# Kernel optimization log

Hardware: AMD Instinct MI355X
Metric: run time of the kernel (lower is better)

## Reference

```python
import jax, jax.numpy as jnp
import numpy as np

B, T, N_EMBD, HEAD = 8, 2048, 1024, 64

def setup_inputs() -> dict:
    key = jax.random.key(0)
    kx, kk, kq, kv = jax.random.split(key, 4)
    x = jax.random.normal(kx, (B, T, N_EMBD), dtype=jnp.float32)
    Wk = jax.random.normal(kk, (HEAD, N_EMBD), dtype=jnp.float32) * 0.02
    Wq = jax.random.normal(kq, (HEAD, N_EMBD), dtype=jnp.float32) * 0.02
    Wv = jax.random.normal(kv, (HEAD, N_EMBD), dtype=jnp.float32) * 0.02
    return {"x": x, "Wk": Wk, "Wq": Wq, "Wv": Wv}

def reference(x, Wk, Wq, Wv):
    # x: [B, T, C]; Linear(n_embd, head_size, bias=False) => x @ W.T
    Bq, Tq, C = x.shape
    q = jnp.einsum('btc,hc->bth', x, Wq)  # [B, T, H]
    k = jnp.einsum('btc,hc->bth', x, Wk)
    v = jnp.einsum('btc,hc->bth', x, Wv)
    # NOTE: source scales by C**0.5 with C = n_embd (not head_size); preserved.
    scale = 1.0 / jnp.sqrt(jnp.float32(C))
    wei = jnp.einsum('bth,bsh->bts', q, k) * scale  # [B, T, T]
    # causal mask: allow key position s <= query position t
    causal = jnp.tril(jnp.ones((Tq, Tq), dtype=bool))
    wei = jnp.where(causal[None, :, :], wei, -jnp.inf)
    wei = jax.nn.softmax(wei, axis=-1)
    # dropout is identity at inference
    out = jnp.einsum('bts,bsh->bth', wei, v)  # [B, T, H]
    return out
```

## Files before the change

### kernel.cpp

```cpp
#include <hip/hip_runtime.h>

#define TB 2048
#define NB 8
#define CEMB 1024
#define HD 64
#define BT (NB*TB)
#define QSCALE 0.04508422f

typedef __attribute__((ext_vector_type(8))) short bf16x8;
typedef __attribute__((ext_vector_type(4))) short bf16x4;
typedef __attribute__((ext_vector_type(4))) float f32x4;

#define MFMA32(a, b, c) __builtin_amdgcn_mfma_f32_16x16x32_bf16(a, b, c, 0, 0, 0)
#define MFMA16(a, b, c) __builtin_amdgcn_mfma_f32_16x16x16bf16_1k(a, b, c, 0, 0, 0)

__device__ inline short f2bf(float f) {
    union { float f; unsigned u; } v; v.f = f;
    unsigned r = v.u + 0x7fffu + ((v.u >> 16) & 1u);
    return (short)(r >> 16);
}
__device__ inline float bf2f(short s) {
    union { unsigned u; float f; } v; v.u = ((unsigned)(unsigned short)s) << 16;
    return v.f;
}
__device__ inline unsigned cvt_pk_bf16(float a, float b) {
    unsigned r;
    asm("v_cvt_pk_bf16_f32 %0, %1, %2" : "=v"(r) : "v"(a), "v"(b));
    return r;
}
__device__ inline bf16x4 pack2(unsigned w0, unsigned w1) {
    union { unsigned u[2]; bf16x4 v; } c; c.u[0] = w0; c.u[1] = w1; return c.v;
}
__device__ inline bf16x8 pack4(unsigned w0, unsigned w1, unsigned w2, unsigned w3) {
    union { unsigned u[4]; bf16x8 v; } c;
    c.u[0] = w0; c.u[1] = w1; c.u[2] = w2; c.u[3] = w3; return c.v;
}
__device__ inline float bflo(unsigned w) {
    union { unsigned u; float f; } v; v.u = w << 16; return v.f;
}
__device__ inline float bfhi(unsigned w) {
    union { unsigned u; float f; } v; v.u = w & 0xffff0000u; return v.f;
}

__global__ __launch_bounds__(256) void wpack(const float* __restrict__ Wk,
                                             const float* __restrict__ Wq,
                                             const float* __restrict__ Wv,
                                             short* __restrict__ W2) {
    int c = blockIdx.x * 256 + threadIdx.x;
    int lane = c & 63, ntk = c >> 6;
    int nt = ntk % 12, kc = ntk / 12;
    int n = nt * 16 + (lane & 15);
    int col = kc * 32 + (lane >> 4) * 8;
    const float* src = (n < 64) ? Wk + n * 1024
                     : (n < 128) ? Wq + (n - 64) * 1024
                                 : Wv + (n - 128) * 1024;
    float4 a = *(const float4*)(src + col);
    float4 b = *(const float4*)(src + col + 4);
    bf16x8 o;
    o[0] = f2bf(a.x); o[1] = f2bf(a.y); o[2] = f2bf(a.z); o[3] = f2bf(a.w);
    o[4] = f2bf(b.x); o[5] = f2bf(b.y); o[6] = f2bf(b.z); o[7] = f2bf(b.w);
    *(bf16x8*)(W2 + (size_t)c * 8) = o;
}

__global__ __launch_bounds__(256, 4) void qkv_proj(const float* __restrict__ x,
                                                   const short* __restrict__ W2,
                                                   short* __restrict__ Qb,
                                                   short* __restrict__ Kb,
                                                   short* __restrict__ Vt) {
    __shared__ uint2 Lred[4][3][3][64];
    int tid = threadIdx.x, wave = tid >> 6, lane = tid & 63;
    int l15 = lane & 15, quad = lane >> 4;
    int m0 = blockIdx.x * 16;

    f32x4 acc[12];
#pragma unroll
    for (int i = 0; i < 12; ++i) acc[i] = f32x4{0.f, 0.f, 0.f, 0.f};

    const float4* xA = (const float4*)(x + (size_t)(m0 + l15) * CEMB + wave * 256) + quad * 2;
    float4 xq[4];
    xq[0] = xA[0]; xq[1] = xA[1]; xq[2] = xA[8]; xq[3] = xA[9];

    const short* wbase = W2 + ((size_t)(wave * 8) * 12 * 64 + lane) * 8;
#pragma unroll
    for (int kc = 0; kc < 8; ++kc) {
        bf16x8 wf[12];
#pragma unroll
        for (int nt = 0; nt < 12; ++nt)
            wf[nt] = *(const bf16x8*)(wbase + (size_t)kc * 6144 + nt * 512);
        int base = (kc & 1) * 2;
        float4 a0 = xq[base], a1 = xq[base + 1];
        if (kc + 2 < 8) {
            xq[base]     = xA[(kc + 2) * 8];
            xq[base + 1] = xA[(kc + 2) * 8 + 1];
        }
        bf16x8 af0 = pack4(cvt_pk_bf16(a0.x, a0.y), cvt_pk_bf16(a0.z, a0.w),
                           cvt_pk_bf16(a1.x, a1.y), cvt_pk_bf16(a1.z, a1.w));
#pragma unroll
        for (int nt = 0; nt < 12; ++nt)
            acc[nt] = MFMA32(af0, wf[nt], acc[nt]);
    }

#pragma unroll
    for (int nt = 0; nt < 12; ++nt) {
        int o = nt / 3;
        if (o != wave) {
            int rank = wave - (wave > o ? 1 : 0);
            uint2 p;
            p.x = cvt_pk_bf16(acc[nt][0], acc[nt][1]);
            p.y = cvt_pk_bf16(acc[nt][2], acc[nt][3]);
            Lred[o][rank][nt % 3][lane] = p;
        }
    }
    __syncthreads();

    int b = blockIdx.x >> 7;
    int sblk32 = (blockIdx.x & 127) >> 1;
    int half = blockIdx.x & 1;
#pragma unroll
    for (int nt = 0; nt < 12; ++nt) {
        if (wave == nt / 3) {
            f32x4 s0 = acc[nt];
#pragma unroll
            for (int rk = 0; rk < 3; ++rk) {
                uint2 p0 = Lred[nt / 3][rk][nt % 3][lane];
                s0[0] += bflo(p0.x); s0[1] += bfhi(p0.x);
                s0[2] += bflo(p0.y); s0[3] += bfhi(p0.y);
            }
            if (nt < 4) {
                int h = nt * 16 + l15;
#pragma unroll
                for (int r = 0; r < 4; ++r)
                    Kb[(size_t)(m0 + quad * 4 + r) * HD + h] = f2bf(s0[r]);
            } else if (nt < 8) {
                int h = (nt - 4) * 16 + l15;
#pragma unroll
                for (int r = 0; r < 4; ++r)
                    Qb[(size_t)(m0 + quad * 4 + r) * HD + h] = f2bf(s0[r] * QSCALE);
            } else {
                int h = (nt - 8) * 16 + l15;
                uint2 v2;
                v2.x = cvt_pk_bf16(s0[0], s0[1]);
                v2.y = cvt_pk_bf16(s0[2], s0[3]);
                *(uint2*)(Vt + ((size_t)((b * 64 + sblk32) * 64 + h)) * 32
                             + quad * 8 + half * 4) = v2;
            }
        }
    }
}

__global__ __launch_bounds__(256) void flash(const short* __restrict__ Qb,
                                             const short* __restrict__ Kb,
                                             const short* __restrict__ Vt,
                                             float* __restrict__ out) {
    __shared__ float Of[4][2][16][68];
    __shared__ float Ml[4][2][16];
    int tid = threadIdx.x, wave = tid >> 6, lane = tid & 63;
    int l15 = lane & 15, quad = lane >> 4;
    int i = blockIdx.x;
    int round = i >> 8, s = i & 255;
    int b = s & 7;
    int g32 = s >> 3;
    int q32 = round ? 63 - g32 : g32;
    int tq0 = q32 * 32;
    size_t bT = (size_t)b * TB;

    const short* qr0 = Qb + (bT + tq0 + l15) * HD;
    const short* qr1 = Qb + (bT + tq0 + 16 + l15) * HD;
    bf16x8 qf00 = *(const bf16x8*)(qr0 + quad * 8);
    bf16x8 qf01 = *(const bf16x8*)(qr0 + 32 + quad * 8);
    bf16x8 qf10 = *(const bf16x8*)(qr1 + quad * 8);
    bf16x8 qf11 = *(const bf16x8*)(qr1 + 32 + quad * 8);

    bf16x4 ones4;
#pragma unroll
    for (int j = 0; j < 4; ++j) ones4[j] = (short)0x3F80;

    f32x4 accO0[4], accO1[4];
#pragma unroll
    for (int k = 0; k < 4; ++k) { accO0[k] = f32x4{0.f,0.f,0.f,0.f}; accO1[k] = f32x4{0.f,0.f,0.f,0.f}; }
    f32x4 accL0 = f32x4{0.f,0.f,0.f,0.f}, accL1 = f32x4{0.f,0.f,0.f,0.f};

    int ntiles = (tq0 + 95) >> 6;
    const short* kbase = Kb + bT * HD;
    const short* vtb = Vt + (size_t)b * 131072;

    int myt = wave;
    if (myt < ntiles) {
        bf16x8 kf[8];
        {
            const short* kr = kbase + (size_t)(myt * 64 + l15) * HD + quad * 8;
#pragma unroll
            for (int st = 0; st < 4; ++st) {
                kf[st * 2]     = *(const bf16x8*)(kr + (size_t)st * 16 * HD);
                kf[st * 2 + 1] = *(const bf16x8*)(kr + (size_t)st * 16 * HD + 32);
            }
        }
        for (; myt < ntiles; myt += 4) {
            int s0 = myt * 64;
            bf16x8 vf8[8];
#pragma unroll
            for (int sb2 = 0; sb2 < 2; ++sb2)
#pragma unroll
                for (int ht = 0; ht < 4; ++ht)
                    vf8[sb2 * 4 + ht] = *(const bf16x8*)(
                        vtb + ((size_t)(((s0 >> 5) + sb2) * 64 + ht * 16 + l15)) * 32 + quad * 8);
            f32x4 sv0[4], sv1[4];
            __builtin_amdgcn_s_setprio(1);
#pragma unroll
            for (int st = 0; st < 4; ++st) {
                f32x4 t0 = f32x4{0.f,0.f,0.f,0.f}, t1 = f32x4{0.f,0.f,0.f,0.f};
                t0 = MFMA32(kf[st * 2], qf00, t0);
                t0 = MFMA32(kf[st * 2 + 1], qf01, t0);
                t1 = MFMA32(kf[st * 2], qf10, t1);
                t1 = MFMA32(kf[st * 2 + 1], qf11, t1);
                sv0[st] = t0; sv1[st] = t1;
            }
            __builtin_amdgcn_s_setprio(0);
            if (myt + 4 < ntiles) {
                const short* kr = kbase + (size_t)(s0 + 256 + l15) * HD + quad * 8;
#pragma unroll
                for (int st = 0; st < 4; ++st) {
                    kf[st * 2]     = *(const bf16x8*)(kr + (size_t)st * 16 * HD);
                    kf[st * 2 + 1] = *(const bf16x8*)(kr + (size_t)st * 16 * HD + 32);
                }
            }
            bf16x4 pk0[4], pk1[4];
            if (s0 + 63 <= tq0) {
#pragma unroll
                for (int st = 0; st < 4; ++st) {
                    unsigned w00 = cvt_pk_bf16(__builtin_amdgcn_exp2f(sv0[st][0]),
                                               __builtin_amdgcn_exp2f(sv0[st][1]));
                    unsigned w01 = cvt_pk_bf16(__builtin_amdgcn_exp2f(sv0[st][2]),
                                               __builtin_amdgcn_exp2f(sv0[st][3]));
                    unsigned w10 = cvt_pk_bf16(__builtin_amdgcn_exp2f(sv1[st][0]),
                                               __builtin_amdgcn_exp2f(sv1[st][1]));
                    unsigned w11 = cvt_pk_bf16(__builtin_amdgcn_exp2f(sv1[st][2]),
                                               __builtin_amdgcn_exp2f(sv1[st][3]));
                    pk0[st] = pack2(w00, w01);
                    pk1[st] = pack2(w10, w11);
                }
            } else {
                int t0g = tq0 + l15, t1g = tq0 + 16 + l15;
#pragma unroll
                for (int st = 0; st < 4; ++st) {
                    bool full0 = (s0 + st * 16 + 15 <= tq0);
                    bool full1 = (s0 + st * 16 + 15 <= tq0 + 16);
                    int sb = s0 + st * 16 + quad * 4;
                    float a0 = (full0 || sb + 0 <= t0g) ? __builtin_amdgcn_exp2f(sv0[st][0]) : 0.f;
                    float a1 = (full0 || sb + 1 <= t0g) ? __builtin_amdgcn_exp2f(sv0[st][1]) : 0.f;
                    float a2 = (full0 || sb + 2 <= t0g) ? __builtin_amdgcn_exp2f(sv0[st][2]) : 0.f;
                    float a3 = (full0 || sb + 3 <= t0g) ? __builtin_amdgcn_exp2f(sv0[st][3]) : 0.f;
                    float c0 = (full1 || sb + 0 <= t1g) ? __builtin_amdgcn_exp2f(sv1[st][0]) : 0.f;
                    float c1 = (full1 || sb + 1 <= t1g) ? __builtin_amdgcn_exp2f(sv1[st][1]) : 0.f;
                    float c2 = (full1 || sb + 2 <= t1g) ? __builtin_amdgcn_exp2f(sv1[st][2]) : 0.f;
                    float c3 = (full1 || sb + 3 <= t1g) ? __builtin_amdgcn_exp2f(sv1[st][3]) : 0.f;
                    pk0[st] = pack2(cvt_pk_bf16(a0, a1), cvt_pk_bf16(a2, a3));
                    pk1[st] = pack2(cvt_pk_bf16(c0, c1), cvt_pk_bf16(c2, c3));
                }
            }
            __builtin_amdgcn_s_setprio(1);
#pragma unroll
            for (int g = 0; g < 4; ++g) {
                accL0 = MFMA16(ones4, pk0[g], accL0);
                accL1 = MFMA16(ones4, pk1[g], accL1);
#pragma unroll
                for (int ht = 0; ht < 4; ++ht) {
                    bf16x8 v = vf8[(g >> 1) * 4 + ht];
                    bf16x4 va;
                    if (g & 1) { va[0] = v[4]; va[1] = v[5]; va[2] = v[6]; va[3] = v[7]; }
                    else       { va[0] = v[0]; va[1] = v[1]; va[2] = v[2]; va[3] = v[3]; }
                    accO0[ht] = MFMA16(va, pk0[g], accO0[ht]);
                    accO1[ht] = MFMA16(va, pk1[g], accO1[ht]);
                }
            }
            __builtin_amdgcn_s_setprio(0);
        }
    }

#pragma unroll
    for (int ht = 0; ht < 4; ++ht) {
        float4 o0, o1;
        o0.x = accO0[ht][0]; o0.y = accO0[ht][1]; o0.z = accO0[ht][2]; o0.w = accO0[ht][3];
        o1.x = accO1[ht][0]; o1.y = accO1[ht][1]; o1.z = accO1[ht][2]; o1.w = accO1[ht][3];
        *(float4*)&Of[wave][0][l15][ht * 16 + quad * 4] = o0;
        *(float4*)&Of[wave][1][l15][ht * 16 + quad * 4] = o1;
    }
    if (quad == 0) { Ml[wave][0][l15] = accL0[0]; Ml[wave][1][l15] = accL1[0]; }
    __syncthreads();

    int row = tid >> 4, c4 = (tid & 15) * 4;
#pragma unroll
    for (int qt = 0; qt < 2; ++qt) {
        float L = Ml[0][qt][row] + Ml[1][qt][row] + Ml[2][qt][row] + Ml[3][qt][row];
        float inv = 1.0f / L;
        float4 p0 = *(const float4*)&Of[0][qt][row][c4];
        float4 p1 = *(const float4*)&Of[1][qt][row][c4];
        float4 p2 = *(const float4*)&Of[2][qt][row][c4];
        float4 p3 = *(const float4*)&Of[3][qt][row][c4];
        float4 o;
        o.x = (p0.x + p1.x + p2.x + p3.x) * inv;
        o.y = (p0.y + p1.y + p2.y + p3.y) * inv;
        o.z = (p0.z + p1.z + p2.z + p3.z) * inv;
        o.w = (p0.w + p1.w + p2.w + p3.w) * inv;
        *(float4*)(out + (bT + tq0 + qt * 16 + row) * HD + c4) = o;
    }
}

extern "C" void kernel_launch(void* const* d_in, const int* in_sizes, int n_in,
                              void* d_out, int out_size, void* d_ws, size_t ws_size,
                              hipStream_t stream) {
    const float* x  = (const float*)d_in[0];
    const float* Wk = (const float*)d_in[1];
    const float* Wq = (const float*)d_in[2];
    const float* Wv = (const float*)d_in[3];
    float* out = (float*)d_out;

    short* W2 = (short*)d_ws;
    short* Qb = W2 + 192 * 1024;
    short* Kb = Qb + (size_t)BT * HD;
    short* Vt = Kb + (size_t)BT * HD;

    wpack<<<96, 256, 0, stream>>>(Wk, Wq, Wv, W2);
    qkv_proj<<<1024, 256, 0, stream>>>(x, W2, Qb, Kb, Vt);
    flash<<<512, 256, 0, stream>>>(Qb, Kb, Vt, out);
}
```

Measured before the change: 134.3 us.

## Restructure QKV projection with LDS double-buffered x tiles and 2D wave tiling

Rewrites the QKV projection so each 512-thread block handles 64 rows. The x tiles are staged into swizzled LDS through async global_load_lds with double buffering, and the 8 waves are split 2x4 across M and N, which removes the split-K cross-wave reduction through shared memory. The aim is to reuse each weight fragment across more rows and to overlap x streaming with MFMA work. In exchange it adds barriers per K step, uses fewer blocks (256), and relies on hand-written vmcnt wait counts.

```diff
diff --git a/kernel.cpp b/kernel.cpp
--- a/kernel.cpp
+++ b/kernel.cpp
@@ -35,11 +35,9 @@
     union { unsigned u[4]; bf16x8 v; } c;
     c.u[0] = w0; c.u[1] = w1; c.u[2] = w2; c.u[3] = w3; return c.v;
 }
-__device__ inline float bflo(unsigned w) {
-    union { unsigned u; float f; } v; v.u = w << 16; return v.f;
-}
-__device__ inline float bfhi(unsigned w) {
-    union { unsigned u; float f; } v; v.u = w & 0xffff0000u; return v.f;
+__device__ inline void gload_lds16(const void* g, void* l) {
+    __builtin_amdgcn_global_load_lds((const __attribute__((address_space(1))) void*)g,
+                                     (__attribute__((address_space(3))) void*)l, 16, 0, 0);
 }
 
 __global__ __launch_bounds__(256) void wpack(const float* __restrict__ Wk,
@@ -62,86 +60,118 @@
     *(bf16x8*)(W2 + (size_t)c * 8) = o;
 }
 
-__global__ __launch_bounds__(256, 4) void qkv_proj(const float* __restrict__ x,
-                                                   const short* __restrict__ W2,
-                                                   short* __restrict__ Qb,
-                                                   short* __restrict__ Kb,
-                                                   short* __restrict__ Vt) {
-    __shared__ uint2 Lred[4][3][3][64];
-    int tid = threadIdx.x, wave = tid >> 6, lane = tid & 63;
+__global__ __launch_bounds__(512) void qkv_proj(const float* __restrict__ x,
+                                                const short* __restrict__ W2,
+                                                short* __restrict__ Qb,
+                                                short* __restrict__ Kb,
+                                                short* __restrict__ Vt) {
+    __shared__ __align__(16) char xbuf[2][16384];
+    int tid = threadIdx.x, wid = tid >> 6, lane = tid & 63;
     int l15 = lane & 15, quad = lane >> 4;
-    int m0 = blockIdx.x * 16;
-
-    f32x4 acc[12];
-#pragma unroll
-    for (int i = 0; i < 12; ++i) acc[i] = f32x4{0.f, 0.f, 0.f, 0.f};
-
-    const float4* xA = (const float4*)(x + (size_t)(m0 + l15) * CEMB + wave * 256) + quad * 2;
-    float4 xq[4];
-    xq[0] = xA[0]; xq[1] = xA[1]; xq[2] = xA[8]; xq[3] = xA[9];
-
-    const short* wbase = W2 + ((size_t)(wave * 8) * 12 * 64 + lane) * 8;
-#pragma unroll
-    for (int kc = 0; kc < 8; ++kc) {
-        bf16x8 wf[12];
-#pragma unroll
-        for (int nt = 0; nt < 12; ++nt)
-            wf[nt] = *(const bf16x8*)(wbase + (size_t)kc * 6144 + nt * 512);
-        int base = (kc & 1) * 2;
-        float4 a0 = xq[base], a1 = xq[base + 1];
-        if (kc + 2 < 8) {
-            xq[base]     = xA[(kc + 2) * 8];
-            xq[base + 1] = xA[(kc + 2) * 8 + 1];
-        }
-        bf16x8 af0 = pack4(cvt_pk_bf16(a0.x, a0.y), cvt_pk_bf16(a0.z, a0.w),
-                           cvt_pk_bf16(a1.x, a1.y), cvt_pk_bf16(a1.z, a1.w));
-#pragma unroll
-        for (int nt = 0; nt < 12; ++nt)
-            acc[nt] = MFMA32(af0, wf[nt], acc[nt]);
-    }
-
-#pragma unroll
-    for (int nt = 0; nt < 12; ++nt) {
-        int o = nt / 3;
-        if (o != wave) {
-            int rank = wave - (wave > o ? 1 : 0);
-            uint2 p;
-            p.x = cvt_pk_bf16(acc[nt][0], acc[nt][1]);
-            p.y = cvt_pk_bf16(acc[nt][2], acc[nt][3]);
-            Lred[o][rank][nt % 3][lane] = p;
-        }
-    }
-    __syncthreads();
-
-    int b = blockIdx.x >> 7;
-    int sblk32 = (blockIdx.x & 127) >> 1;
-    int half = blockIdx.x & 1;
-#pragma unroll
-    for (int nt = 0; nt < 12; ++nt) {
-        if (wave == nt / 3) {
-            f32x4 s0 = acc[nt];
-#pragma unroll
-            for (int rk = 0; rk < 3; ++rk) {
-                uint2 p0 = Lred[nt / 3][rk][nt % 3][lane];
-                s0[0] += bflo(p0.x); s0[1] += bfhi(p0.x);
-                s0[2] += bflo(p0.y); s0[3] += bfhi(p0.y);
-            }
-            if (nt < 4) {
-                int h = nt * 16 + l15;
+    int mgrp = wid >> 2;
+    int ngrp = wid & 3;
+    int m0 = blockIdx.x * 64;
+
+    f32x4 acc[2][3];
+#pragma unroll
+    for (int i = 0; i < 2; ++i)
+#pragma unroll
+        for (int j = 0; j < 3; ++j) acc[i][j] = f32x4{0.f, 0.f, 0.f, 0.f};
+
+    int ld4 = lane >> 4;
+    const char* gs0; const char* gs1;
+    {
+        int r0 = (wid * 2) * 4 + ld4;
+        int r1 = (wid * 2 + 1) * 4 + ld4;
+        int sz0 = ((r0 & 3) << 5) | ((r0 & 4) << 2);
+        int sz1 = ((r1 & 3) << 5) | ((r1 & 4) << 2);
+        gs0 = (const char*)x + ((size_t)(m0 + r0) << 12) + ((l15 * 16) ^ sz0);
+        gs1 = (const char*)x + ((size_t)(m0 + r1) << 12) + ((l15 * 16) ^ sz1);
+    }
+#define STAGE(bsel, t) do { \
+        gload_lds16(gs0 + (t) * 256, &xbuf[bsel][(wid * 2) * 1024]);     \
+        gload_lds16(gs1 + (t) * 256, &xbuf[bsel][(wid * 2 + 1) * 1024]); } while (0)
+
+    int lrowA = mgrp * 32 + l15;
+    int szr = ((lrowA & 3) << 5) | ((lrowA & 4) << 2);
+    int baseA = lrowA * 256;
+    int baseB = baseA + 4096;
+
+    const short* wnt = W2 + (size_t)(ngrp * 3) * 512 + (size_t)lane * 8;
+
+    STAGE(0, 0);
+    for (int t = 0; t < 16; ++t) {
+        bf16x8 wfj[3][2];
+        {
+            const short* ws = wnt + (size_t)(2 * t) * 6144;
+#pragma unroll
+            for (int j = 0; j < 3; ++j) {
+                wfj[j][0] = *(const bf16x8*)(ws + j * 512);
+                wfj[j][1] = *(const bf16x8*)(ws + j * 512 + 6144);
+            }
+        }
+        if (t < 15) {
+            STAGE((t + 1) & 1, t + 1);
+            asm volatile("s_waitcnt vmcnt(8)" ::: "memory");
+        } else {
+            asm volatile("s_waitcnt vmcnt(6)" ::: "memory");
+        }
+        __builtin_amdgcn_s_barrier();
+
+        const char* bp = &xbuf[t & 1][0];
+        bf16x8 af[2][2];
+#pragma unroll
+        for (int kh = 0; kh < 2; ++kh) {
+            int b0 = kh * 128 + quad * 32;
+            float4 a0 = *(const float4*)(bp + baseA + ((b0) ^ szr));
+            float4 a1 = *(const float4*)(bp + baseA + ((b0 + 16) ^ szr));
+            float4 c0 = *(const float4*)(bp + baseB + ((b0) ^ szr));
+            float4 c1 = *(const float4*)(bp + baseB + ((b0 + 16) ^ szr));
+            af[0][kh] = pack4(cvt_pk_bf16(a0.x, a0.y), cvt_pk_bf16(a0.z, a0.w),
+                              cvt_pk_bf16(a1.x, a1.y), cvt_pk_bf16(a1.z, a1.w));
+            af[1][kh] = pack4(cvt_pk_bf16(c0.x, c0.y), cvt_pk_bf16(c0.z, c0.w),
+                              cvt_pk_bf16(c1.x, c1.y), cvt_pk_bf16(c1.z, c1.w));
+        }
+#pragma unroll
+        for (int kh = 0; kh < 2; ++kh)
+#pragma unroll
+            for (int j = 0; j < 3; ++j) {
+                acc[0][j] = MFMA32(af[0][kh], wfj[j][kh], acc[0][j]);
+                acc[1][j] = MFMA32(af[1][kh], wfj[j][kh], acc[1][j]);
+            }
+        __builtin_amdgcn_s_barrier();
+    }
+#undef STAGE
+
+    int blk = blockIdx.x;
+    int bb = blk >> 5;
+    int inb = blk & 31;
+#pragma unroll
+    for (int j = 0; j < 3; ++j) {
+        int gnt = ngrp * 3 + j;
+#pragma unroll
+        for (int mt = 0; mt < 2; ++mt) {
+            int gmt = mgrp * 2 + mt;
+            f32x4 s0 = acc[mt][j];
+            int row0 = m0 + gmt * 16 + quad * 4;
+            if (gnt < 4) {
+                int h = gnt * 16 + l15;
 #pragma unroll
                 for (int r = 0; r < 4; ++r)
-                    Kb[(size_t)(m0 + quad * 4 + r) * HD + h] = f2bf(s0[r]);
-            } else if (nt < 8) {
-                int h = (nt - 4) * 16 + l15;
+                    Kb[(size_t)(row0 + r) * HD + h] = f2bf(s0[r]);
+            } else if (gnt < 8) {
+                int h = (gnt - 4) * 16 + l15;
 #pragma unroll
                 for (int r = 0; r < 4; ++r)
-                    Qb[(size_t)(m0 + quad * 4 + r) * HD + h] = f2bf(s0[r] * QSCALE);
+                    Qb[(size_t)(row0 + r) * HD + h] = f2bf(s0[r] * QSCALE);
             } else {
-                int h = (nt - 8) * 16 + l15;
+                int h = (gnt - 8) * 16 + l15;
+                int sblk32 = inb * 2 + (gmt >> 1);
+                int half = gmt & 1;
                 uint2 v2;
                 v2.x = cvt_pk_bf16(s0[0], s0[1]);
                 v2.y = cvt_pk_bf16(s0[2], s0[3]);
-                *(uint2*)(Vt + ((size_t)((b * 64 + sblk32) * 64 + h)) * 32
+                *(uint2*)(Vt + ((size_t)((bb * 64 + sblk32) * 64 + h)) * 32
                              + quad * 8 + half * 4) = v2;
             }
         }
@@ -321,6 +351,6 @@
     short* Vt = Kb + (size_t)BT * HD;
 
     wpack<<<96, 256, 0, stream>>>(Wk, Wq, Wv, W2);
-    qkv_proj<<<1024, 256, 0, stream>>>(x, W2, Qb, Kb, Vt);
+    qkv_proj<<<256, 512, 0, stream>>>(x, W2, Qb, Kb, Vt);
     flash<<<512, 256, 0, stream>>>(Qb, Kb, Vt, out);
 }
```

New measurement: 136.4 us. About the same (+1.6%).
